# Optimization experiments

Hardware: AMD Instinct MI355X
Metric: run time of the kernel (lower is better)

Reference implementation:

```python
import jax, jax.numpy as jnp
import numpy as np

N = 32          # objects in the (single) image
P = N * (N - 1) # relation pairs
D = 256         # self.dim
M = 14          # mask_size / pooler resolution
OC = 151        # obj classes
RC = 51         # rel classes
RED = D // 4    # attention gate reduction


def setup_inputs() -> dict:
    key = jax.random.key(0)
    ks = jax.random.split(key, 32)
    # all ordered pairs i != j
    ii, jj = np.meshgrid(np.arange(N), np.arange(N), indexing='ij')
    keep = ii != jj
    rel_pair_idxs = jnp.asarray(np.stack([ii[keep], jj[keep]], 1), jnp.int32)  # [P,2]
    # valid xyxy boxes in an 800x600 image
    x1 = jax.random.uniform(ks[0], (N,)) * 600.0
    y1 = jax.random.uniform(ks[1], (N,)) * 400.0
    w = jax.random.uniform(ks[2], (N,)) * 180.0 + 20.0
    h = jax.random.uniform(ks[3], (N,)) * 180.0 + 20.0
    bboxes = jnp.stack([x1, y1, x1 + w, y1 + h], 1).astype(jnp.float32)
    roi_features = jax.random.normal(ks[4], (N, 4096), jnp.float32)
    predict_logits = jax.random.normal(ks[5], (N, OC), jnp.float32)
    union_features = jax.random.normal(ks[6], (P, D, M, M), jnp.float32)
    s = 0.02
    p = dict(
        roi_features=roi_features, bboxes=bboxes, predict_logits=predict_logits,
        union_features=union_features, rel_pair_idxs=rel_pair_idxs,
        W_emb1=jax.random.normal(ks[7], (4096 + OC + 4, D)) * s, b_emb1=jnp.zeros((D,)),
        W_emb2=jax.random.normal(ks[8], (D, D)) * s, b_emb2=jnp.zeros((D,)),
        # stacked SE-attention gates: 0=sbj, 1=obj, 2=bg
        att_fc1_w=jax.random.normal(ks[9], (3, D, RED)) * s, att_fc1_b=jnp.zeros((3, RED)),
        att_fc2_w=jax.random.normal(ks[10], (3, RED, D)) * s, att_fc2_b=jnp.zeros((3, D)),
        W_c1=jax.random.normal(ks[11], (3 * D, D)) * s, b_c1=jnp.zeros((D,)),
        W_c2=jax.random.normal(ks[12], (D, D)) * s, b_c2=jnp.zeros((D,)),
        W_gcn=jax.random.normal(ks[13], (D, D)) * s, b_gcn=jnp.zeros((D,)),
        W_objp=jax.random.normal(ks[14], (D, OC)) * s, b_objp=jnp.zeros((OC,)),
        W_relp=jax.random.normal(ks[15], (D, RC)) * s, b_relp=jnp.zeros((RC,)),
    )
    return p


def _rect_masks(x0, y0, x1, y1):
    # mask[p, r, c] = 1 iff x0<=r<x1 and y0<=c<y1  (matches torch slice write)
    r = jnp.arange(M, dtype=jnp.float32)
    rm = (r[None, :] >= x0[:, None]) & (r[None, :] < x1[:, None])  # [P,M]
    cm = (r[None, :] >= y0[:, None]) & (r[None, :] < y1[:, None])  # [P,M]
    return (rm[:, :, None] & cm[:, None, :]).astype(jnp.float32)   # [P,M,M]


def _masking(union_features, bboxes, pairs):
    sb = bboxes[pairs[:, 0]]  # [P,4]
    ob = bboxes[pairs[:, 1]]
    ux1 = jnp.minimum(sb[:, 0], ob[:, 0])
    uy1 = jnp.minimum(sb[:, 1], ob[:, 1])
    x = jnp.stack([sb[:, 0], sb[:, 2], ob[:, 0], ob[:, 2]], 1) - ux1[:, None]
    y = jnp.stack([sb[:, 1], sb[:, 3], ob[:, 1], ob[:, 3]], 1) - uy1[:, None]
    xr = M / jnp.maximum(x[:, 1], x[:, 3])
    yr = M / jnp.maximum(y[:, 1], y[:, 3])
    xp = jnp.round(x * xr[:, None])
    yp = jnp.round(y * yr[:, None])
    sm = _rect_masks(xp[:, 0], yp[:, 0], xp[:, 1], yp[:, 1])[:, None]  # [P,1,M,M]
    om = _rect_masks(xp[:, 2], yp[:, 2], xp[:, 3], yp[:, 3])[:, None]
    bm = jnp.clip(1.0 - sm - om, 0.0, 1.0)
    return union_features * sm, union_features * om, union_features * bm


def _att_gate(x, w1, b1, w2, b2):
    # SE-style channel attention gate
    s = x.mean((2, 3))                                        # [P,D]
    g = jax.nn.sigmoid(jax.nn.relu(s @ w1 + b1) @ w2 + b2)    # [P,D]
    return x * g[:, :, None, None]


def _adjacency(pairs):
    o2o = jnp.zeros((N, N)).at[pairs[:, 0], pairs[:, 1]].set(1.0)
    ar = jnp.arange(P)
    o2r = jnp.zeros((N, P)).at[pairs[:, 0], ar].set(1.0).at[pairs[:, 1], ar].set(1.0)
    top = jnp.concatenate([o2o, o2r], 1)                     # [N, N+P]
    bot = jnp.concatenate([o2r.T, jnp.zeros((P, P))], 1)     # [P, N+P]
    adj = jnp.concatenate([top, bot], 0)
    return adj + jnp.eye(N + P)


def reference(roi_features, bboxes, predict_logits, union_features, rel_pair_idxs,
              W_emb1, b_emb1, W_emb2, b_emb2,
              att_fc1_w, att_fc1_b, att_fc2_w, att_fc2_b,
              W_c1, b_c1, W_c2, b_c2, W_gcn, b_gcn,
              W_objp, b_objp, W_relp, b_relp):
    pairs = rel_pair_idxs
    # object embedding
    obj_in = jnp.concatenate([roi_features, predict_logits, bboxes], 1)  # [N,4251]
    obj_feats = jax.nn.relu(obj_in @ W_emb1 + b_emb1) @ W_emb2 + b_emb2  # [N,D]
    # masking + attention gates + global avg pool
    sbj, obj, bg = _masking(union_features, bboxes, pairs)
    sbj = _att_gate(sbj, att_fc1_w[0], att_fc1_b[0], att_fc2_w[0], att_fc2_b[0]).mean((2, 3))
    obj = _att_gate(obj, att_fc1_w[1], att_fc1_b[1], att_fc2_w[1], att_fc2_b[1]).mean((2, 3))
    bg = _att_gate(bg, att_fc1_w[2], att_fc1_b[2], att_fc2_w[2], att_fc2_b[2]).mean((2, 3))
    # relational embedding (compose)
    rel = jnp.concatenate([sbj, obj, bg], 1)                 # [P,3D]
    rel_feats = jax.nn.relu(rel @ W_c1 + b_c1) @ W_c2 + b_c2  # [P,D]
    # GCN over object+relation graph (row-normalized adjacency, residual)
    adj = _adjacency(pairs)
    feats = jnp.concatenate([obj_feats, rel_feats], 0)        # [N+P,D]
    norm_adj = adj / adj.sum(1, keepdims=True)
    gcn_out = jax.nn.relu(norm_adj @ (feats @ W_gcn) + b_gcn) + feats
    obj_dists = gcn_out[:N] @ W_objp + b_objp                 # [N,OC]
    rel_dists = gcn_out[N:] @ W_relp + b_relp                 # [P,RC]
    return obj_dists, rel_dists
```

## Files before the change

### kernel.cpp

```cpp
#include <hip/hip_runtime.h>
#include <cstdint>
#include <cstddef>

#define NOBJ 32
#define NP   992
#define DD   256
#define SP   196
#define OC   151
#define RC   51
#define RED  64
#define KIN  4251
#define CH   128
#define KPC  34

#define OFF_PART   0u
#define OFF_OBJF   1048576u
#define OFF_SALL   1056768u
#define OFF_RELF   1818624u
#define OFF_H      2072576u
#define OFF_W2T    2334720u
#define OFF_WC1T   2400256u
#define OFF_WC2T   2596864u
#define OFF_WGT    2662400u
#define OFF_FC1WT  2727936u
#define OFF_FC2WT  2777088u
#define OFF_WOPT   2826240u
#define OFF_WRPT   2864896u

#define TR_TOT 543232

#define TCH  32
#define NTIL 8
#define TF4  1568

__global__ void __launch_bounds__(256, 5)
k_pre(const float* __restrict__ uf,
      const float* __restrict__ bbox,
      const int* __restrict__ pairs,
      const float* __restrict__ roi,
      const float* __restrict__ logits,
      const float* __restrict__ W1,
      const float* __restrict__ W2,  const float* __restrict__ Wc1,
      const float* __restrict__ Wc2, const float* __restrict__ Wg,
      const float* __restrict__ f1w, const float* __restrict__ f2w,
      const float* __restrict__ Wop, const float* __restrict__ Wrp,
      float* __restrict__ sAll, float* __restrict__ part,
      float* __restrict__ W2T,  float* __restrict__ Wc1T,
      float* __restrict__ Wc2T, float* __restrict__ WgT,
      float* __restrict__ f1wT, float* __restrict__ f2wT,
      float* __restrict__ WopT, float* __restrict__ WrpT) {
  const int b = blockIdx.x, t = threadIdx.x;
  if (b < NP) {
    const int p = b;
    __shared__ __align__(16) float buf[TCH * SP + 28];
    __shared__ __align__(16) float mS[224];
    __shared__ __align__(16) float mO[224];
    __shared__ __align__(16) float mB[224];
    if (t < 224) {
      float sm = 0.f, om = 0.f, bm = 0.f;
      if (t < SP) {
        int si = pairs[2 * p], oi = pairs[2 * p + 1];
        float sx1 = bbox[si * 4 + 0], sy1 = bbox[si * 4 + 1];
        float sx2 = bbox[si * 4 + 2], sy2 = bbox[si * 4 + 3];
        float ox1 = bbox[oi * 4 + 0], oy1 = bbox[oi * 4 + 1];
        float ox2 = bbox[oi * 4 + 2], oy2 = bbox[oi * 4 + 3];
        float ux = fminf(sx1, ox1), uy = fminf(sy1, oy1);
        float xr = 14.f / fmaxf(sx2 - ux, ox2 - ux);
        float yr = 14.f / fmaxf(sy2 - uy, oy2 - uy);
        float xs0 = rintf((sx1 - ux) * xr), xs1 = rintf((sx2 - ux) * xr);
        float xo0 = rintf((ox1 - ux) * xr), xo1 = rintf((ox2 - ux) * xr);
        float ys0 = rintf((sy1 - uy) * yr), ys1 = rintf((sy2 - uy) * yr);
        float yo0 = rintf((oy1 - uy) * yr), yo1 = rintf((oy2 - uy) * yr);
        int a = t / 14, bb = t - a * 14;
        float fa = (float)a, fb = (float)bb;
        sm = (fa >= xs0 && fa < xs1 && fb >= ys0 && fb < ys1) ? 1.f : 0.f;
        om = (fa >= xo0 && fa < xo1 && fb >= yo0 && fb < yo1) ? 1.f : 0.f;
        bm = fminf(fmaxf(1.f - sm - om, 0.f), 1.f);
      }
      mS[t] = sm; mO[t] = om; mB[t] = bm;
    }
    if (t < 28) buf[TCH * SP + t] = 0.f;
    const float4* base4 = (const float4*)(uf + (size_t)p * (DD * SP));
    {
      const float4* src = base4 + t;
      float4* dst = (float4*)buf + t;
      dst[0] = src[0];     dst[256] = src[256];   dst[512] = src[512];
      dst[768] = src[768]; dst[1024] = src[1024]; dst[1280] = src[1280];
      if (t < 32) dst[1536] = src[1536];
    }
    __syncthreads();
    const int cl = t >> 3, o = t & 7;
    const float* row = buf + cl * SP + o * 28;
    const float* msp = mS + o * 28;
    const float* mop = mO + o * 28;
    const float* mbp = mB + o * 28;
    const float inv = 1.f / 196.f;
    float4 s0, s1, s2, s3, s4, s5, s6 = {0.f, 0.f, 0.f, 0.f};
#pragma unroll 1
    for (int ti = 0; ti < NTIL; ++ti) {
      if (ti < NTIL - 1) {
        const float4* src = base4 + (ti + 1) * TF4 + t;
        s0 = src[0];     s1 = src[256];   s2 = src[512];
        s3 = src[768];   s4 = src[1024];  s5 = src[1280];
        if (t < 32) s6 = src[1536];
      }
      float aS = 0.f, aO = 0.f, aB = 0.f;
#pragma unroll
      for (int j = 0; j < 7; ++j) {
        float4 v = *(const float4*)&row[4 * j];
        float4 x = *(const float4*)&msp[4 * j];
        float4 y = *(const float4*)&mop[4 * j];
        float4 z = *(const float4*)&mbp[4 * j];
        aS += v.x * x.x + v.y * x.y + v.z * x.z + v.w * x.w;
        aO += v.x * y.x + v.y * y.y + v.z * y.z + v.w * y.w;
        aB += v.x * z.x + v.y * z.y + v.z * z.z + v.w * z.w;
      }
      aS += __shfl_xor(aS, 1); aS += __shfl_xor(aS, 2); aS += __shfl_xor(aS, 4);
      aO += __shfl_xor(aO, 1); aO += __shfl_xor(aO, 2); aO += __shfl_xor(aO, 4);
      aB += __shfl_xor(aB, 1); aB += __shfl_xor(aB, 2); aB += __shfl_xor(aB, 4);
      const int ch = ti * TCH + cl;
      if (o == 0)      sAll[(size_t)p * 768 + ch]       = aS * inv;
      else if (o == 1) sAll[(size_t)p * 768 + 256 + ch] = aO * inv;
      else if (o == 2) sAll[(size_t)p * 768 + 512 + ch] = aB * inv;
      if (ti < NTIL - 1) {
        __syncthreads();
        float4* dst = (float4*)buf + t;
        dst[0] = s0;     dst[256] = s1;   dst[512] = s2;
        dst[768] = s3;   dst[1024] = s4;  dst[1280] = s5;
        if (t < 32) dst[1536] = s6;
        __syncthreads();
      }
    }
  } else if (b < NP + CH) {
    const int chunk = b - NP;
    int k0 = chunk * KPC;
    int k1 = k0 + KPC; if (k1 > KIN) k1 = KIN;
    float acc[NOBJ];
#pragma unroll
    for (int i = 0; i < NOBJ; ++i) acc[i] = 0.f;
#pragma unroll 2
    for (int k = k0; k < k1; ++k) {
      float w = W1[(size_t)k * DD + t];
      const float* xp; int stride;
      if (k < 4096)            { xp = roi    + k;               stride = 4096; }
      else if (k < 4096 + OC)  { xp = logits + (k - 4096);      stride = OC;   }
      else                     { xp = bbox   + (k - 4096 - OC); stride = 4;    }
#pragma unroll
      for (int i = 0; i < NOBJ; ++i) { acc[i] += xp[0] * w; xp += stride; }
    }
    float* pout = part + (size_t)chunk * (NOBJ * DD) + t;
#pragma unroll
    for (int i = 0; i < NOBJ; ++i) pout[i * DD] = acc[i];
  } else {
    for (int o = (b - NP - CH) * 256 + t; o < TR_TOT; o += 256 * 256) {
      float v; float* dst;
      if (o < 65536)       { int q = o;          v = W2 [(q & 255) * 256 + (q >> 8)]; dst = W2T  + q; }
      else if (o < 262144) { int q = o - 65536;  int c = q / 768, k = q - c * 768;
                             v = Wc1[k * 256 + c];                                    dst = Wc1T + q; }
      else if (o < 327680) { int q = o - 262144; v = Wc2[(q & 255) * 256 + (q >> 8)]; dst = Wc2T + q; }
      else if (o < 393216) { int q = o - 327680; v = Wg [(q & 255) * 256 + (q >> 8)]; dst = WgT  + q; }
      else if (o < 442368) { int q = o - 393216;
                             v = f1w[(q >> 14) * 16384 + (q & 255) * 64 + ((q >> 8) & 63)];
                             dst = f1wT + q; }
      else if (o < 491520) { int q = o - 442368;
                             v = f2w[(q >> 14) * 16384 + (q & 63) * 256 + ((q >> 6) & 255)];
                             dst = f2wT + q; }
      else if (o < 530176) { int q = o - 491520; v = Wop[(q & 255) * OC + (q >> 8)];  dst = WopT + q; }
      else                 { int q = o - 530176; v = Wrp[(q & 255) * RC + (q >> 8)];  dst = WrpT + q; }
      *dst = v;
    }
  }
}

__global__ void __launch_bounds__(512, 1)
k_mid2(const float* __restrict__ sAll,
       const float* __restrict__ f1wT, const float* __restrict__ f1b,
       const float* __restrict__ f2wT, const float* __restrict__ f2b,
       const float* __restrict__ Wc1T, const float* __restrict__ bc1,
       const float* __restrict__ Wc2T, const float* __restrict__ bc2,
       const float* __restrict__ WgT,
       const float* __restrict__ part, const float* __restrict__ b1,
       const float* __restrict__ W2T,  const float* __restrict__ b2,
       float* __restrict__ relf, float* __restrict__ objf,
       float* __restrict__ H) {
  const int b = blockIdx.x, t = threadIdx.x;
  const int h = t >> 8, tt = t & 255;
  __shared__ __align__(16) float sg[4][768];
  __shared__ __align__(16) float ha[4][192];
  __shared__ __align__(16) float h2[4][256];
  __shared__ __align__(16) float red[2][4][256];
  if (b < NP / 4) {
    const int p0 = b * 4;
    {
      const float4* src = (const float4*)(sAll + (size_t)p0 * 768);
      float4* dst = (float4*)&sg[0][0];
      for (int j = t; j < 768; j += 512) dst[j] = src[j];
    }
    __syncthreads();
    if (tt < 192) {
      const float4* w4 = (const float4*)(f1wT + tt * 256 + h * 128);
      const int sb = (tt >> 6) * 256 + h * 128;
      float a0 = 0, a1 = 0, a2 = 0, a3 = 0;
#pragma unroll 8
      for (int j = 0; j < 32; ++j) {
        float4 wv = w4[j];
        float4 s0 = *(const float4*)&sg[0][sb + 4 * j];
        float4 s1 = *(const float4*)&sg[1][sb + 4 * j];
        float4 s2 = *(const float4*)&sg[2][sb + 4 * j];
        float4 s3 = *(const float4*)&sg[3][sb + 4 * j];
        a0 += s0.x * wv.x + s0.y * wv.y + s0.z * wv.z + s0.w * wv.w;
        a1 += s1.x * wv.x + s1.y * wv.y + s1.z * wv.z + s1.w * wv.w;
        a2 += s2.x * wv.x + s2.y * wv.y + s2.z * wv.z + s2.w * wv.w;
        a3 += s3.x * wv.x + s3.y * wv.y + s3.z * wv.z + s3.w * wv.w;
      }
      red[h][0][tt] = a0; red[h][1][tt] = a1; red[h][2][tt] = a2; red[h][3][tt] = a3;
    }
    __syncthreads();
    if (h == 0 && tt < 192) {
      float bb = f1b[tt];
#pragma unroll
      for (int p = 0; p < 4; ++p)
        ha[p][tt] = fmaxf(red[0][p][tt] + red[1][p][tt] + bb, 0.f);
    }
    __syncthreads();
    for (int br = 0; br < 3; ++br) {
      const float4* w4 = (const float4*)(f2wT + br * 16384 + tt * 64 + h * 32);
      const int hb = br * 64 + h * 32;
      float a0 = 0, a1 = 0, a2 = 0, a3 = 0;
#pragma unroll
      for (int j = 0; j < 8; ++j) {
        float4 wv = w4[j];
        float4 v0 = *(const float4*)&ha[0][hb + 4 * j];
        float4 v1 = *(const float4*)&ha[1][hb + 4 * j];
        float4 v2 = *(const float4*)&ha[2][hb + 4 * j];
        float4 v3 = *(const float4*)&ha[3][hb + 4 * j];
        a0 += v0.x * wv.x + v0.y * wv.y + v0.z * wv.z + v0.w * wv.w;
        a1 += v1.x * wv.x + v1.y * wv.y + v1.z * wv.z + v1.w * wv.w;
        a2 += v2.x * wv.x + v2.y * wv.y + v2.z * wv.z + v2.w * wv.w;
        a3 += v3.x * wv.x + v3.y * wv.y + v3.z * wv.z + v3.w * wv.w;
      }
      red[h][0][tt] = a0; red[h][1][tt] = a1; red[h][2][tt] = a2; red[h][3][tt] = a3;
      __syncthreads();
      if (h == 0) {
        float bb = f2b[br * 256 + tt];
#pragma unroll
        for (int p = 0; p < 4; ++p) {
          float g = 1.f / (1.f + expf(-(red[0][p][tt] + red[1][p][tt] + bb)));
          sg[p][br * 256 + tt] *= g;
        }
      }
      __syncthreads();
    }
    {
      const float4* w4 = (const float4*)(Wc1T + (size_t)tt * 768 + h * 384);
      const int gb = h * 384;
      float a0 = 0, a1 = 0, a2 = 0, a3 = 0;
#pragma unroll 8
      for (int j = 0; j < 96; ++j) {
        float4 wv = w4[j];
        float4 g0 = *(const float4*)&sg[0][gb + 4 * j];
        float4 g1 = *(const float4*)&sg[1][gb + 4 * j];
        float4 g2 = *(const float4*)&sg[2][gb + 4 * j];
        float4 g3 = *(const float4*)&sg[3][gb + 4 * j];
        a0 += g0.x * wv.x + g0.y * wv.y + g0.z * wv.z + g0.w * wv.w;
        a1 += g1.x * wv.x + g1.y * wv.y + g1.z * wv.z + g1.w * wv.w;
        a2 += g2.x * wv.x + g2.y * wv.y + g2.z * wv.z + g2.w * wv.w;
        a3 += g3.x * wv.x + g3.y * wv.y + g3.z * wv.z + g3.w * wv.w;
      }
      red[h][0][tt] = a0; red[h][1][tt] = a1; red[h][2][tt] = a2; red[h][3][tt] = a3;
    }
    __syncthreads();
    if (h == 0) {
      float bb = bc1[tt];
#pragma unroll
      for (int p = 0; p < 4; ++p)
        h2[p][tt] = fmaxf(red[0][p][tt] + red[1][p][tt] + bb, 0.f);
    }
    __syncthreads();
    {
      const float4* w4 = (const float4*)(Wc2T + (size_t)tt * 256 + h * 128);
      const int hb = h * 128;
      float a0 = 0, a1 = 0, a2 = 0, a3 = 0;
#pragma unroll 8
      for (int j = 0; j < 32; ++j) {
        float4 wv = w4[j];
        float4 v0 = *(const float4*)&h2[0][hb + 4 * j];
        float4 v1 = *(const float4*)&h2[1][hb + 4 * j];
        float4 v2 = *(const float4*)&h2[2][hb + 4 * j];
        float4 v3 = *(const float4*)&h2[3][hb + 4 * j];
        a0 += v0.x * wv.x + v0.y * wv.y + v0.z * wv.z + v0.w * wv.w;
        a1 += v1.x * wv.x + v1.y * wv.y + v1.z * wv.z + v1.w * wv.w;
        a2 += v2.x * wv.x + v2.y * wv.y + v2.z * wv.z + v2.w * wv.w;
        a3 += v3.x * wv.x + v3.y * wv.y + v3.z * wv.z + v3.w * wv.w;
      }
      red[h][0][tt] = a0; red[h][1][tt] = a1; red[h][2][tt] = a2; red[h][3][tt] = a3;
    }
    __syncthreads();
    if (h == 0) {
      float bb = bc2[tt];
#pragma unroll
      for (int p = 0; p < 4; ++p) {
        float v = red[0][p][tt] + red[1][p][tt] + bb;
        relf[(size_t)(p0 + p) * DD + tt] = v;
        sg[p][tt] = v;
      }
    }
    __syncthreads();
    {
      const float4* w4 = (const float4*)(WgT + (size_t)tt * 256 + h * 128);
      const int hb = h * 128;
      float a0 = 0, a1 = 0, a2 = 0, a3 = 0;
#pragma unroll 8
      for (int j = 0; j < 32; ++j) {
        float4 wv = w4[j];
        float4 v0 = *(const float4*)&sg[0][hb + 4 * j];
        float4 v1 = *(const float4*)&sg[1][hb + 4 * j];
        float4 v2 = *(const float4*)&sg[2][hb + 4 * j];
        float4 v3 = *(const float4*)&sg[3][hb + 4 * j];
        a0 += v0.x * wv.x + v0.y * wv.y + v0.z * wv.z + v0.w * wv.w;
        a1 += v1.x * wv.x + v1.y * wv.y + v1.z * wv.z + v1.w * wv.w;
        a2 += v2.x * wv.x + v2.y * wv.y + v2.z * wv.z + v2.w * wv.w;
        a3 += v3.x * wv.x + v3.y * wv.y + v3.z * wv.z + v3.w * wv.w;
      }
      red[h][0][tt] = a0; red[h][1][tt] = a1; red[h][2][tt] = a2; red[h][3][tt] = a3;
    }
    __syncthreads();
    if (h == 0) {
#pragma unroll
      for (int p = 0; p < 4; ++p)
        H[(size_t)(NOBJ + p0 + p) * DD + tt] = red[0][p][tt] + red[1][p][tt];
    }
  } else {
    const int r = (b - NP / 4) * 2 + h;
    float s[8];
#pragma unroll
    for (int u = 0; u < 8; ++u) s[u] = 0.f;
#pragma unroll
    for (int c0 = 0; c0 < CH; c0 += 8) {
#pragma unroll
      for (int u = 0; u < 8; ++u)
        s[u] += part[(size_t)(c0 + u) * (NOBJ * DD) + r * DD + tt];
    }
    float tot = ((s[0] + s[1]) + (s[2] + s[3])) + ((s[4] + s[5]) + (s[6] + s[7]));
    h2[h][tt] = fmaxf(tot + b1[tt], 0.f);
    __syncthreads();
    {
      const float4* w4 = (const float4*)(W2T + (size_t)tt * DD);
      const float* hp = &h2[h][0];
      float a0 = 0, a1 = 0, a2 = 0, a3 = 0;
#pragma unroll 8
      for (int j = 0; j < 64; ++j) {
        float4 wv = w4[j];
        float4 hv = *(const float4*)&hp[4 * j];
        a0 += hv.x * wv.x; a1 += hv.y * wv.y; a2 += hv.z * wv.z; a3 += hv.w * wv.w;
      }
      float v = (a0 + a1) + (a2 + a3) + b2[tt];
      objf[r * DD + tt] = v;
      sg[h][tt] = v;
    }
    __syncthreads();
    {
      const float4* w4 = (const float4*)(WgT + (size_t)tt * DD);
      const float* hp = &sg[h][0];
      float a0 = 0, a1 = 0, a2 = 0, a3 = 0;
#pragma unroll 8
      for (int j = 0; j < 64; ++j) {
        float4 wv = w4[j];
        float4 hv = *(const float4*)&hp[4 * j];
        a0 += hv.x * wv.x; a1 += hv.y * wv.y; a2 += hv.z * wv.z; a3 += hv.w * wv.w;
      }
      H[(size_t)r * DD + tt] = (a0 + a1) + (a2 + a3);
    }
  }
}

__global__ void __launch_bounds__(1024, 1)
k_heads(const float* __restrict__ H, const float* __restrict__ objf,
        const float* __restrict__ relf, const int* __restrict__ pairs,
        const float* __restrict__ bg,
        const float* __restrict__ WopT, const float* __restrict__ bop,
        const float* __restrict__ WrpT, const float* __restrict__ brp,
        float* __restrict__ out) {
  const int b = blockIdx.x, t = threadIdx.x;
  const int p = t >> 8, tt = t & 255;
  if (b < NP / 4) {
    __shared__ __align__(16) float gr[4][DD];
    __shared__ float red[4][4][64];
    const int r = b * 4 + p;
    int si = pairs[2 * r], oi = pairs[2 * r + 1];
    float hsum = H[si * DD + tt] + H[oi * DD + tt] + H[(size_t)(NOBJ + r) * DD + tt];
    gr[p][tt] = fmaxf(hsum * (1.f / 3.f) + bg[tt], 0.f) + relf[(size_t)r * DD + tt];
    __syncthreads();
    const int q = tt >> 6, c = tt & 63;
    float a = 0.f;
    if (c < RC) {
      const float4* w4 = (const float4*)(WrpT + c * 256 + q * 64);
#pragma unroll
      for (int j = 0; j < 16; ++j) {
        float4 wv = w4[j];
        float4 gv = *(const float4*)&gr[p][q * 64 + 4 * j];
        a += gv.x * wv.x + gv.y * wv.y + gv.z * wv.z + gv.w * wv.w;
      }
    }
    red[p][q][c] = a;
    __syncthreads();
    if (tt < RC)
      out[NOBJ * OC + (size_t)r * RC + tt] =
          red[p][0][tt] + red[p][1][tt] + red[p][2][tt] + red[p][3][tt] + brp[tt];
  } else {
    const int i = b - NP / 4;
    const int slice = p;
    __shared__ int2 pr[NP];
    __shared__ float red2[4][DD];
    __shared__ __align__(16) float gro[DD];
    const int2* p2 = (const int2*)pairs;
    for (int r = t; r < NP; r += 1024) pr[r] = p2[r];
    __syncthreads();
    float acc = 0.f;
    if (slice == 0) {
#pragma unroll 8
      for (int j = 0; j < NOBJ; ++j) acc += H[j * DD + tt];
    }
    const int rbeg = slice * 248;
#pragma unroll 8
    for (int r = rbeg; r < rbeg + 248; ++r) {
      int2 q = pr[r];
      float v = H[(size_t)(NOBJ + r) * DD + tt];
      if (q.x == i || q.y == i) acc += v;
    }
    red2[slice][tt] = acc;
    __syncthreads();
    if (t < DD) {
      float pre = (red2[0][t] + red2[1][t] + red2[2][t] + red2[3][t]) * (1.f / 94.f);
      gro[t] = fmaxf(pre + bg[t], 0.f) + objf[i * DD + t];
    }
    __syncthreads();
    float hsum = 0.f;
    if (tt < OC) {
      const float4* w4 = (const float4*)(WopT + tt * 256 + slice * 64);
#pragma unroll
      for (int j = 0; j < 16; ++j) {
        float4 wv = w4[j];
        float4 gv = *(const float4*)&gro[slice * 64 + 4 * j];
        hsum += gv.x * wv.x + gv.y * wv.y + gv.z * wv.z + gv.w * wv.w;
      }
    }
    red2[slice][tt] = hsum;
    __syncthreads();
    if (t < OC)
      out[i * OC + t] = red2[0][t] + red2[1][t] + red2[2][t] + red2[3][t] + bop[t];
  }
}

extern "C" void kernel_launch(void* const* d_in, const int* in_sizes, int n_in,
                              void* d_out, int out_size, void* d_ws, size_t ws_size,
                              hipStream_t stream) {
  const float* roi   = (const float*)d_in[0];
  const float* bbox  = (const float*)d_in[1];
  const float* logit = (const float*)d_in[2];
  const float* uf    = (const float*)d_in[3];
  const int*   pairs = (const int*)d_in[4];
  const float* W1    = (const float*)d_in[5];
  const float* b1    = (const float*)d_in[6];
  const float* W2    = (const float*)d_in[7];
  const float* b2    = (const float*)d_in[8];
  const float* fc1w  = (const float*)d_in[9];
  const float* fc1b  = (const float*)d_in[10];
  const float* fc2w  = (const float*)d_in[11];
  const float* fc2b  = (const float*)d_in[12];
  const float* Wc1   = (const float*)d_in[13];
  const float* bc1   = (const float*)d_in[14];
  const float* Wc2   = (const float*)d_in[15];
  const float* bc2   = (const float*)d_in[16];
  const float* Wg    = (const float*)d_in[17];
  const float* bg    = (const float*)d_in[18];
  const float* Wop   = (const float*)d_in[19];
  const float* bop   = (const float*)d_in[20];
  const float* Wrp   = (const float*)d_in[21];
  const float* brp   = (const float*)d_in[22];

  float* ws    = (float*)d_ws;
  float* part  = ws + OFF_PART;
  float* objf  = ws + OFF_OBJF;
  float* sAll  = ws + OFF_SALL;
  float* relf  = ws + OFF_RELF;
  float* Hbuf  = ws + OFF_H;
  float* W2T   = ws + OFF_W2T;
  float* Wc1T  = ws + OFF_WC1T;
  float* Wc2T  = ws + OFF_WC2T;
  float* WgT   = ws + OFF_WGT;
  float* f1wT  = ws + OFF_FC1WT;
  float* f2wT  = ws + OFF_FC2WT;
  float* WopT  = ws + OFF_WOPT;
  float* WrpT  = ws + OFF_WRPT;
  float* out   = (float*)d_out;

  k_pre<<<NP + CH + 256, 256, 0, stream>>>(uf, bbox, pairs, roi, logit, W1,
                                           W2, Wc1, Wc2, Wg, fc1w, fc2w, Wop, Wrp,
                                           sAll, part, W2T, Wc1T, Wc2T, WgT,
                                           f1wT, f2wT, WopT, WrpT);
  k_mid2<<<NP / 4 + 16, 512, 0, stream>>>(sAll, f1wT, fc1b, f2wT, fc2b,
                                          Wc1T, bc1, Wc2T, bc2, WgT,
                                          part, b1, W2T, b2, relf, objf, Hbuf);
  k_heads<<<NP / 4 + NOBJ, 1024, 0, stream>>>(Hbuf, objf, relf, pairs, bg,
                                              WopT, bop, WrpT, brp, out);
}
```

Measured before the change: 498.6 us.

## Read union features directly from global memory instead of LDS staging

The masked-pooling phase stops staging each pair's union-feature tile into shared memory with a register-prefetch double buffer. Each group of four threads now reduces one channel row straight from global memory with float4 loads, and the reduction shuffle shrinks from three levels to two. This removes about 25 KB of LDS per block and the barriers between tiles, which should allow higher occupancy and remove the sync overhead. In exchange, the global loads are strided per channel and less coalesced, and there is no explicit prefetch. The launch-bounds occupancy hint drops from 5 to 4.

```diff
diff --git a/kernel.cpp b/kernel.cpp
--- a/kernel.cpp
+++ b/kernel.cpp
@@ -29,11 +29,7 @@
 
 #define TR_TOT 543232
 
-#define TCH  32
-#define NTIL 8
-#define TF4  1568
-
-__global__ void __launch_bounds__(256, 5)
+__global__ void __launch_bounds__(256, 4)
 k_pre(const float* __restrict__ uf,
       const float* __restrict__ bbox,
       const int* __restrict__ pairs,
@@ -52,7 +48,6 @@
   const int b = blockIdx.x, t = threadIdx.x;
   if (b < NP) {
     const int p = b;
-    __shared__ __align__(16) float buf[TCH * SP + 28];
     __shared__ __align__(16) float mS[224];
     __shared__ __align__(16) float mO[224];
     __shared__ __align__(16) float mB[224];
@@ -79,57 +74,42 @@
       }
       mS[t] = sm; mO[t] = om; mB[t] = bm;
     }
-    if (t < 28) buf[TCH * SP + t] = 0.f;
-    const float4* base4 = (const float4*)(uf + (size_t)p * (DD * SP));
-    {
-      const float4* src = base4 + t;
-      float4* dst = (float4*)buf + t;
-      dst[0] = src[0];     dst[256] = src[256];   dst[512] = src[512];
-      dst[768] = src[768]; dst[1024] = src[1024]; dst[1280] = src[1280];
-      if (t < 32) dst[1536] = src[1536];
-    }
-    __syncthreads();
-    const int cl = t >> 3, o = t & 7;
-    const float* row = buf + cl * SP + o * 28;
-    const float* msp = mS + o * 28;
-    const float* mop = mO + o * 28;
-    const float* mbp = mB + o * 28;
+    __syncthreads();
+    const int g = t >> 2, i = t & 3;
     const float inv = 1.f / 196.f;
-    float4 s0, s1, s2, s3, s4, s5, s6 = {0.f, 0.f, 0.f, 0.f};
+    const float* base = uf + (size_t)p * (DD * SP);
+    const size_t pout = (size_t)p * 768;
 #pragma unroll 1
-    for (int ti = 0; ti < NTIL; ++ti) {
-      if (ti < NTIL - 1) {
-        const float4* src = base4 + (ti + 1) * TF4 + t;
-        s0 = src[0];     s1 = src[256];   s2 = src[512];
-        s3 = src[768];   s4 = src[1024];  s5 = src[1280];
-        if (t < 32) s6 = src[1536];
-      }
+    for (int c0 = 0; c0 < DD; c0 += 64) {
+      const int c = c0 + g;
+      const float* row = base + c * SP;
       float aS = 0.f, aO = 0.f, aB = 0.f;
 #pragma unroll
-      for (int j = 0; j < 7; ++j) {
-        float4 v = *(const float4*)&row[4 * j];
-        float4 x = *(const float4*)&msp[4 * j];
-        float4 y = *(const float4*)&mop[4 * j];
-        float4 z = *(const float4*)&mbp[4 * j];
+      for (int j = 0; j < 12; ++j) {
+        const int q = 4 * j + i;
+        float4 v = *(const float4*)(row + 4 * q);
+        float4 x = *(const float4*)&mS[4 * q];
+        float4 y = *(const float4*)&mO[4 * q];
+        float4 z = *(const float4*)&mB[4 * q];
         aS += v.x * x.x + v.y * x.y + v.z * x.z + v.w * x.w;
         aO += v.x * y.x + v.y * y.y + v.z * y.z + v.w * y.w;
         aB += v.x * z.x + v.y * z.y + v.z * z.z + v.w * z.w;
       }
-      aS += __shfl_xor(aS, 1); aS += __shfl_xor(aS, 2); aS += __shfl_xor(aS, 4);
-      aO += __shfl_xor(aO, 1); aO += __shfl_xor(aO, 2); aO += __shfl_xor(aO, 4);
-      aB += __shfl_xor(aB, 1); aB += __shfl_xor(aB, 2); aB += __shfl_xor(aB, 4);
-      const int ch = ti * TCH + cl;
-      if (o == 0)      sAll[(size_t)p * 768 + ch]       = aS * inv;
-      else if (o == 1) sAll[(size_t)p * 768 + 256 + ch] = aO * inv;
-      else if (o == 2) sAll[(size_t)p * 768 + 512 + ch] = aB * inv;
-      if (ti < NTIL - 1) {
-        __syncthreads();
-        float4* dst = (float4*)buf + t;
-        dst[0] = s0;     dst[256] = s1;   dst[512] = s2;
-        dst[768] = s3;   dst[1024] = s4;  dst[1280] = s5;
-        if (t < 32) dst[1536] = s6;
-        __syncthreads();
-      }
+      if (i == 0) {
+        float4 v = *(const float4*)(row + 192);
+        float4 x = *(const float4*)&mS[192];
+        float4 y = *(const float4*)&mO[192];
+        float4 z = *(const float4*)&mB[192];
+        aS += v.x * x.x + v.y * x.y + v.z * x.z + v.w * x.w;
+        aO += v.x * y.x + v.y * y.y + v.z * y.z + v.w * y.w;
+        aB += v.x * z.x + v.y * z.y + v.z * z.z + v.w * z.w;
+      }
+      aS += __shfl_xor(aS, 1); aS += __shfl_xor(aS, 2);
+      aO += __shfl_xor(aO, 1); aO += __shfl_xor(aO, 2);
+      aB += __shfl_xor(aB, 1); aB += __shfl_xor(aB, 2);
+      if (i == 0)      sAll[pout + c]       = aS * inv;
+      else if (i == 1) sAll[pout + 256 + c] = aO * inv;
+      else if (i == 2) sAll[pout + 512 + c] = aB * inv;
     }
   } else if (b < NP + CH) {
     const int chunk = b - NP;
```

Measured after the change: 539.8 us. 1.08x slower.

## Read weights in native layout in k_mid2, drop transpose pre-pass

Applied to the files above, without the earlier changes.

Removes the transpose of most dense weights (W2, Wc1, Wc2, Wg, gate fc1/fc2) from k_pre. k_mid2 now reads those weights in their original row-major layout, with coalesced float4 column reads per lane. Work is remapped so each 64-lane wavefront owns one relation pair, with 256-thread blocks instead of 512 and no cross-half reduction buffer. This cuts transpose traffic and the extra workspace writes and reads, but each wavefront now re-reads every weight matrix for a single pair, so weight reuse per block drops.

```diff
diff --git a/kernel.cpp b/kernel.cpp
--- a/kernel.cpp
+++ b/kernel.cpp
@@ -27,7 +27,7 @@
 #define OFF_WOPT   2826240u
 #define OFF_WRPT   2864896u
 
-#define TR_TOT 543232
+#define TR_TOT 51712
 
 #define TCH  32
 #define NTIL 8
@@ -40,14 +40,8 @@
       const float* __restrict__ roi,
       const float* __restrict__ logits,
       const float* __restrict__ W1,
-      const float* __restrict__ W2,  const float* __restrict__ Wc1,
-      const float* __restrict__ Wc2, const float* __restrict__ Wg,
-      const float* __restrict__ f1w, const float* __restrict__ f2w,
       const float* __restrict__ Wop, const float* __restrict__ Wrp,
       float* __restrict__ sAll, float* __restrict__ part,
-      float* __restrict__ W2T,  float* __restrict__ Wc1T,
-      float* __restrict__ Wc2T, float* __restrict__ WgT,
-      float* __restrict__ f1wT, float* __restrict__ f2wT,
       float* __restrict__ WopT, float* __restrict__ WrpT) {
   const int b = blockIdx.x, t = threadIdx.x;
   if (b < NP) {
@@ -152,186 +146,143 @@
 #pragma unroll
     for (int i = 0; i < NOBJ; ++i) pout[i * DD] = acc[i];
   } else {
-    for (int o = (b - NP - CH) * 256 + t; o < TR_TOT; o += 256 * 256) {
+    for (int o = (b - NP - CH) * 256 + t; o < TR_TOT; o += 64 * 256) {
       float v; float* dst;
-      if (o < 65536)       { int q = o;          v = W2 [(q & 255) * 256 + (q >> 8)]; dst = W2T  + q; }
-      else if (o < 262144) { int q = o - 65536;  int c = q / 768, k = q - c * 768;
-                             v = Wc1[k * 256 + c];                                    dst = Wc1T + q; }
-      else if (o < 327680) { int q = o - 262144; v = Wc2[(q & 255) * 256 + (q >> 8)]; dst = Wc2T + q; }
-      else if (o < 393216) { int q = o - 327680; v = Wg [(q & 255) * 256 + (q >> 8)]; dst = WgT  + q; }
-      else if (o < 442368) { int q = o - 393216;
-                             v = f1w[(q >> 14) * 16384 + (q & 255) * 64 + ((q >> 8) & 63)];
-                             dst = f1wT + q; }
-      else if (o < 491520) { int q = o - 442368;
-                             v = f2w[(q >> 14) * 16384 + (q & 63) * 256 + ((q >> 6) & 255)];
-                             dst = f2wT + q; }
-      else if (o < 530176) { int q = o - 491520; v = Wop[(q & 255) * OC + (q >> 8)];  dst = WopT + q; }
-      else                 { int q = o - 530176; v = Wrp[(q & 255) * RC + (q >> 8)];  dst = WrpT + q; }
+      if (o < 38656) { int q = o;         v = Wop[(q & 255) * OC + (q >> 8)]; dst = WopT + q; }
+      else           { int q = o - 38656; v = Wrp[(q & 255) * RC + (q >> 8)]; dst = WrpT + q; }
       *dst = v;
     }
   }
 }
 
-__global__ void __launch_bounds__(512, 1)
+__global__ void __launch_bounds__(256, 4)
 k_mid2(const float* __restrict__ sAll,
-       const float* __restrict__ f1wT, const float* __restrict__ f1b,
-       const float* __restrict__ f2wT, const float* __restrict__ f2b,
-       const float* __restrict__ Wc1T, const float* __restrict__ bc1,
-       const float* __restrict__ Wc2T, const float* __restrict__ bc2,
-       const float* __restrict__ WgT,
+       const float* __restrict__ f1w, const float* __restrict__ f1b,
+       const float* __restrict__ f2w, const float* __restrict__ f2b,
+       const float* __restrict__ Wc1, const float* __restrict__ bc1,
+       const float* __restrict__ Wc2, const float* __restrict__ bc2,
+       const float* __restrict__ Wg,
        const float* __restrict__ part, const float* __restrict__ b1,
-       const float* __restrict__ W2T,  const float* __restrict__ b2,
+       const float* __restrict__ W2,  const float* __restrict__ b2,
        float* __restrict__ relf, float* __restrict__ objf,
        float* __restrict__ H) {
   const int b = blockIdx.x, t = threadIdx.x;
-  const int h = t >> 8, tt = t & 255;
   __shared__ __align__(16) float sg[4][768];
   __shared__ __align__(16) float ha[4][192];
   __shared__ __align__(16) float h2[4][256];
-  __shared__ __align__(16) float red[2][4][256];
+  __shared__ __align__(16) float hob[256];
+  __shared__ __align__(16) float eob[256];
   if (b < NP / 4) {
-    const int p0 = b * 4;
-    {
-      const float4* src = (const float4*)(sAll + (size_t)p0 * 768);
-      float4* dst = (float4*)&sg[0][0];
-      for (int j = t; j < 768; j += 512) dst[j] = src[j];
-    }
-    __syncthreads();
-    if (tt < 192) {
-      const float4* w4 = (const float4*)(f1wT + tt * 256 + h * 128);
-      const int sb = (tt >> 6) * 256 + h * 128;
-      float a0 = 0, a1 = 0, a2 = 0, a3 = 0;
+    const int w = t >> 6, l = t & 63;
+    const int r = b * 4 + w;
+    {
+      const float4* src = (const float4*)(sAll + (size_t)r * 768);
+      float4* dst = (float4*)&sg[w][0];
+      dst[l] = src[l]; dst[64 + l] = src[64 + l]; dst[128 + l] = src[128 + l];
+    }
+    __syncthreads();
+    {
+      float a0 = 0.f, a1 = 0.f, a2 = 0.f;
+      const float* w0 = f1w + l;
+      const float* w1 = f1w + 16384 + l;
+      const float* w2 = f1w + 32768 + l;
+#pragma unroll 4
+      for (int d4 = 0; d4 < 64; ++d4) {
+        float4 x0 = *((const float4*)&sg[w][0]   + d4);
+        float4 x1 = *((const float4*)&sg[w][256] + d4);
+        float4 x2 = *((const float4*)&sg[w][512] + d4);
+        int d = 4 * d4;
+        a0 += x0.x * w0[d * 64] + x0.y * w0[(d + 1) * 64] +
+              x0.z * w0[(d + 2) * 64] + x0.w * w0[(d + 3) * 64];
+        a1 += x1.x * w1[d * 64] + x1.y * w1[(d + 1) * 64] +
+              x1.z * w1[(d + 2) * 64] + x1.w * w1[(d + 3) * 64];
+        a2 += x2.x * w2[d * 64] + x2.y * w2[(d + 1) * 64] +
+              x2.z * w2[(d + 2) * 64] + x2.w * w2[(d + 3) * 64];
+      }
+      ha[w][l]       = fmaxf(a0 + f1b[l], 0.f);
+      ha[w][64 + l]  = fmaxf(a1 + f1b[64 + l], 0.f);
+      ha[w][128 + l] = fmaxf(a2 + f1b[128 + l], 0.f);
+    }
+    __syncthreads();
+#pragma unroll
+    for (int br = 0; br < 3; ++br) {
+      float ax = 0.f, ay = 0.f, az = 0.f, aw = 0.f;
+      const float4* wp = (const float4*)(f2w + br * 16384) + l;
 #pragma unroll 8
-      for (int j = 0; j < 32; ++j) {
-        float4 wv = w4[j];
-        float4 s0 = *(const float4*)&sg[0][sb + 4 * j];
-        float4 s1 = *(const float4*)&sg[1][sb + 4 * j];
-        float4 s2 = *(const float4*)&sg[2][sb + 4 * j];
-        float4 s3 = *(const float4*)&sg[3][sb + 4 * j];
-        a0 += s0.x * wv.x + s0.y * wv.y + s0.z * wv.z + s0.w * wv.w;
-        a1 += s1.x * wv.x + s1.y * wv.y + s1.z * wv.z + s1.w * wv.w;
-        a2 += s2.x * wv.x + s2.y * wv.y + s2.z * wv.z + s2.w * wv.w;
-        a3 += s3.x * wv.x + s3.y * wv.y + s3.z * wv.z + s3.w * wv.w;
-      }
-      red[h][0][tt] = a0; red[h][1][tt] = a1; red[h][2][tt] = a2; red[h][3][tt] = a3;
-    }
-    __syncthreads();
-    if (h == 0 && tt < 192) {
-      float bb = f1b[tt];
-#pragma unroll
-      for (int p = 0; p < 4; ++p)
-        ha[p][tt] = fmaxf(red[0][p][tt] + red[1][p][tt] + bb, 0.f);
-    }
-    __syncthreads();
-    for (int br = 0; br < 3; ++br) {
-      const float4* w4 = (const float4*)(f2wT + br * 16384 + tt * 64 + h * 32);
-      const int hb = br * 64 + h * 32;
-      float a0 = 0, a1 = 0, a2 = 0, a3 = 0;
-#pragma unroll
-      for (int j = 0; j < 8; ++j) {
-        float4 wv = w4[j];
-        float4 v0 = *(const float4*)&ha[0][hb + 4 * j];
-        float4 v1 = *(const float4*)&ha[1][hb + 4 * j];
-        float4 v2 = *(const float4*)&ha[2][hb + 4 * j];
-        float4 v3 = *(const float4*)&ha[3][hb + 4 * j];
-        a0 += v0.x * wv.x + v0.y * wv.y + v0.z * wv.z + v0.w * wv.w;
-        a1 += v1.x * wv.x + v1.y * wv.y + v1.z * wv.z + v1.w * wv.w;
-        a2 += v2.x * wv.x + v2.y * wv.y + v2.z * wv.z + v2.w * wv.w;
-        a3 += v3.x * wv.x + v3.y * wv.y + v3.z * wv.z + v3.w * wv.w;
-      }
-      red[h][0][tt] = a0; red[h][1][tt] = a1; red[h][2][tt] = a2; red[h][3][tt] = a3;
-      __syncthreads();
-      if (h == 0) {
-        float bb = f2b[br * 256 + tt];
-#pragma unroll
-        for (int p = 0; p < 4; ++p) {
-          float g = 1.f / (1.f + expf(-(red[0][p][tt] + red[1][p][tt] + bb)));
-          sg[p][br * 256 + tt] *= g;
-        }
-      }
-      __syncthreads();
-    }
-    {
-      const float4* w4 = (const float4*)(Wc1T + (size_t)tt * 768 + h * 384);
-      const int gb = h * 384;
-      float a0 = 0, a1 = 0, a2 = 0, a3 = 0;
-#pragma unroll 8
-      for (int j = 0; j < 96; ++j) {
-        float4 wv = w4[j];
-        float4 g0 = *(const float4*)&sg[0][gb + 4 * j];
-        float4 g1 = *(const float4*)&sg[1][gb + 4 * j];
-        float4 g2 = *(const float4*)&sg[2][gb + 4 * j];
-        float4 g3 = *(const float4*)&sg[3][gb + 4 * j];
-        a0 += g0.x * wv.x + g0.y * wv.y + g0.z * wv.z + g0.w * wv.w;
-        a1 += g1.x * wv.x + g1.y * wv.y + g1.z * wv.z + g1.w * wv.w;
-        a2 += g2.x * wv.x + g2.y * wv.y + g2.z * wv.z + g2.w * wv.w;
-        a3 += g3.x * wv.x + g3.y * wv.y + g3.z * wv.z + g3.w * wv.w;
-      }
-      red[h][0][tt] = a0; red[h][1][tt] = a1; red[h][2][tt] = a2; red[h][3][tt] = a3;
-    }
-    __syncthreads();
-    if (h == 0) {
-      float bb = bc1[tt];
-#pragma unroll
-      for (int p = 0; p < 4; ++p)
-        h2[p][tt] = fmaxf(red[0][p][tt] + red[1][p][tt] + bb, 0.f);
-    }
-    __syncthreads();
-    {
-      const float4* w4 = (const float4*)(Wc2T + (size_t)tt * 256 + h * 128);
-      const int hb = h * 128;
-      float a0 = 0, a1 = 0, a2 = 0, a3 = 0;
-#pragma unroll 8
-      for (int j = 0; j < 32; ++j) {
-        float4 wv = w4[j];
-        float4 v0 = *(const float4*)&h2[0][hb + 4 * j];
-        float4 v1 = *(const float4*)&h2[1][hb + 4 * j];
-        float4 v2 = *(const float4*)&h2[2][hb + 4 * j];
-        float4 v3 = *(const float4*)&h2[3][hb + 4 * j];
-        a0 += v0.x * wv.x + v0.y * wv.y + v0.z * wv.z + v0.w * wv.w;
-        a1 += v1.x * wv.x + v1.y * wv.y + v1.z * wv.z + v1.w * wv.w;
-        a2 += v2.x * wv.x + v2.y * wv.y + v2.z * wv.z + v2.w * wv.w;
-        a3 += v3.x * wv.x + v3.y * wv.y + v3.z * wv.z + v3.w * wv.w;
-      }
-      red[h][0][tt] = a0; red[h][1][tt] = a1; red[h][2][tt] = a2; red[h][3][tt] = a3;
-    }
-    __syncthreads();
-    if (h == 0) {
-      float bb = bc2[tt];
-#pragma unroll
-      for (int p = 0; p < 4; ++p) {
-        float v = red[0][p][tt] + red[1][p][tt] + bb;
-        relf[(size_t)(p0 + p) * DD + tt] = v;
-        sg[p][tt] = v;
-      }
-    }
-    __syncthreads();
-    {
-      const float4* w4 = (const float4*)(WgT + (size_t)tt * 256 + h * 128);
-      const int hb = h * 128;
-      float a0 = 0, a1 = 0, a2 = 0, a3 = 0;
-#pragma unroll 8
-      for (int j = 0; j < 32; ++j) {
-        float4 wv = w4[j];
-        float4 v0 = *(const float4*)&sg[0][hb + 4 * j];
-        float4 v1 = *(const float4*)&sg[1][hb + 4 * j];
-        float4 v2 = *(const float4*)&sg[2][hb + 4 * j];
-        float4 v3 = *(const float4*)&sg[3][hb + 4 * j];
-        a0 += v0.x * wv.x + v0.y * wv.y + v0.z * wv.z + v0.w * wv.w;
-        a1 += v1.x * wv.x + v1.y * wv.y + v1.z * wv.z + v1.w * wv.w;
-        a2 += v2.x * wv.x + v2.y * wv.y + v2.z * wv.z + v2.w * wv.w;
-        a3 += v3.x * wv.x + v3.y * wv.y + v3.z * wv.z + v3.w * wv.w;
-      }
-      red[h][0][tt] = a0; red[h][1][tt] = a1; red[h][2][tt] = a2; red[h][3][tt] = a3;
-    }
-    __syncthreads();
-    if (h == 0) {
-#pragma unroll
-      for (int p = 0; p < 4; ++p)
-        H[(size_t)(NOBJ + p0 + p) * DD + tt] = red[0][p][tt] + red[1][p][tt];
+      for (int red = 0; red < 64; ++red) {
+        float x = ha[w][br * 64 + red];
+        float4 wv = wp[red * 64];
+        ax += x * wv.x; ay += x * wv.y; az += x * wv.z; aw += x * wv.w;
+      }
+      float4 bb = *((const float4*)(f2b + br * 256) + l);
+      float4 sv = *((float4*)&sg[w][br * 256] + l);
+      sv.x *= 1.f / (1.f + expf(-(ax + bb.x)));
+      sv.y *= 1.f / (1.f + expf(-(ay + bb.y)));
+      sv.z *= 1.f / (1.f + expf(-(az + bb.z)));
+      sv.w *= 1.f / (1.f + expf(-(aw + bb.w)));
+      *((float4*)&sg[w][br * 256] + l) = sv;
+    }
+    __syncthreads();
+    {
+      float ax = 0.f, ay = 0.f, az = 0.f, aw = 0.f;
+      const float4* wp = (const float4*)Wc1 + l;
+#pragma unroll 4
+      for (int k4 = 0; k4 < 192; ++k4) {
+        float4 x = *((const float4*)&sg[w][0] + k4);
+        int k = 4 * k4;
+        float4 v0 = wp[(size_t)k * 64], v1 = wp[(size_t)(k + 1) * 64];
+        float4 v2 = wp[(size_t)(k + 2) * 64], v3 = wp[(size_t)(k + 3) * 64];
+        ax += x.x * v0.x + x.y * v1.x + x.z * v2.x + x.w * v3.x;
+        ay += x.x * v0.y + x.y * v1.y + x.z * v2.y + x.w * v3.y;
+        az += x.x * v0.z + x.y * v1.z + x.z * v2.z + x.w * v3.z;
+        aw += x.x * v0.w + x.y * v1.w + x.z * v2.w + x.w * v3.w;
+      }
+      float4 bb = *((const float4*)bc1 + l);
+      float4 hv;
+      hv.x = fmaxf(ax + bb.x, 0.f); hv.y = fmaxf(ay + bb.y, 0.f);
+      hv.z = fmaxf(az + bb.z, 0.f); hv.w = fmaxf(aw + bb.w, 0.f);
+      *((float4*)&h2[w][0] + l) = hv;
+    }
+    __syncthreads();
+    {
+      float ax = 0.f, ay = 0.f, az = 0.f, aw = 0.f;
+      const float4* wp = (const float4*)Wc2 + l;
+#pragma unroll 4
+      for (int k4 = 0; k4 < 64; ++k4) {
+        float4 x = *((const float4*)&h2[w][0] + k4);
+        int k = 4 * k4;
+        float4 v0 = wp[k * 64], v1 = wp[(k + 1) * 64];
+        float4 v2 = wp[(k + 2) * 64], v3 = wp[(k + 3) * 64];
+        ax += x.x * v0.x + x.y * v1.x + x.z * v2.x + x.w * v3.x;
+        ay += x.x * v0.y + x.y * v1.y + x.z * v2.y + x.w * v3.y;
+        az += x.x * v0.z + x.y * v1.z + x.z * v2.z + x.w * v3.z;
+        aw += x.x * v0.w + x.y * v1.w + x.z * v2.w + x.w * v3.w;
+      }
+      float4 bb = *((const float4*)bc2 + l);
+      float4 v; v.x = ax + bb.x; v.y = ay + bb.y; v.z = az + bb.z; v.w = aw + bb.w;
+      *(float4*)(relf + (size_t)r * DD + 4 * l) = v;
+      *((float4*)&sg[w][0] + l) = v;
+    }
+    __syncthreads();
+    {
+      float ax = 0.f, ay = 0.f, az = 0.f, aw = 0.f;
+      const float4* wp = (const float4*)Wg + l;
+#pragma unroll 4
+      for (int k4 = 0; k4 < 64; ++k4) {
+        float4 x = *((const float4*)&sg[w][0] + k4);
+        int k = 4 * k4;
+        float4 v0 = wp[k * 64], v1 = wp[(k + 1) * 64];
+        float4 v2 = wp[(k + 2) * 64], v3 = wp[(k + 3) * 64];
+        ax += x.x * v0.x + x.y * v1.x + x.z * v2.x + x.w * v3.x;
+        ay += x.x * v0.y + x.y * v1.y + x.z * v2.y + x.w * v3.y;
+        az += x.x * v0.z + x.y * v1.z + x.z * v2.z + x.w * v3.z;
+        aw += x.x * v0.w + x.y * v1.w + x.z * v2.w + x.w * v3.w;
+      }
+      float4 v; v.x = ax; v.y = ay; v.z = az; v.w = aw;
+      *(float4*)(H + (size_t)(NOBJ + r) * DD + 4 * l) = v;
     }
   } else {
-    const int r = (b - NP / 4) * 2 + h;
+    const int i = b - NP / 4;
     float s[8];
 #pragma unroll
     for (int u = 0; u < 8; ++u) s[u] = 0.f;
@@ -339,37 +290,35 @@
     for (int c0 = 0; c0 < CH; c0 += 8) {
 #pragma unroll
       for (int u = 0; u < 8; ++u)
-        s[u] += part[(size_t)(c0 + u) * (NOBJ * DD) + r * DD + tt];
+        s[u] += part[(size_t)(c0 + u) * (NOBJ * DD) + i * DD + t];
     }
     float tot = ((s[0] + s[1]) + (s[2] + s[3])) + ((s[4] + s[5]) + (s[6] + s[7]));
-    h2[h][tt] = fmaxf(tot + b1[tt], 0.f);
-    __syncthreads();
-    {
-      const float4* w4 = (const float4*)(W2T + (size_t)tt * DD);
-      const float* hp = &h2[h][0];
-      float a0 = 0, a1 = 0, a2 = 0, a3 = 0;
-#pragma unroll 8
-      for (int j = 0; j < 64; ++j) {
-        float4 wv = w4[j];
-        float4 hv = *(const float4*)&hp[4 * j];
-        a0 += hv.x * wv.x; a1 += hv.y * wv.y; a2 += hv.z * wv.z; a3 += hv.w * wv.w;
-      }
-      float v = (a0 + a1) + (a2 + a3) + b2[tt];
-      objf[r * DD + tt] = v;
-      sg[h][tt] = v;
-    }
-    __syncthreads();
-    {
-      const float4* w4 = (const float4*)(WgT + (size_t)tt * DD);
-      const float* hp = &sg[h][0];
-      float a0 = 0, a1 = 0, a2 = 0, a3 = 0;
-#pragma unroll 8
-      for (int j = 0; j < 64; ++j) {
-        float4 wv = w4[j];
-        float4 hv = *(const float4*)&hp[4 * j];
-        a0 += hv.x * wv.x; a1 += hv.y * wv.y; a2 += hv.z * wv.z; a3 += hv.w * wv.w;
-      }
-      H[(size_t)r * DD + tt] = (a0 + a1) + (a2 + a3);
+    hob[t] = fmaxf(tot + b1[t], 0.f);
+    __syncthreads();
+    {
+      float a = 0.f;
+#pragma unroll 4
+      for (int k4 = 0; k4 < 64; ++k4) {
+        float4 hv = *((const float4*)hob + k4);
+        int k = 4 * k4;
+        a += hv.x * W2[k * 256 + t]       + hv.y * W2[(k + 1) * 256 + t]
+           + hv.z * W2[(k + 2) * 256 + t] + hv.w * W2[(k + 3) * 256 + t];
+      }
+      float v = a + b2[t];
+      objf[i * DD + t] = v;
+      eob[t] = v;
+    }
+    __syncthreads();
+    {
+      float a = 0.f;
+#pragma unroll 4
+      for (int k4 = 0; k4 < 64; ++k4) {
+        float4 ev = *((const float4*)eob + k4);
+        int k = 4 * k4;
+        a += ev.x * Wg[k * 256 + t]       + ev.y * Wg[(k + 1) * 256 + t]
+           + ev.z * Wg[(k + 2) * 256 + t] + ev.w * Wg[(k + 3) * 256 + t];
+      }
+      H[(size_t)i * DD + t] = a;
     }
   }
 }
@@ -485,23 +434,15 @@
   float* sAll  = ws + OFF_SALL;
   float* relf  = ws + OFF_RELF;
   float* Hbuf  = ws + OFF_H;
-  float* W2T   = ws + OFF_W2T;
-  float* Wc1T  = ws + OFF_WC1T;
-  float* Wc2T  = ws + OFF_WC2T;
-  float* WgT   = ws + OFF_WGT;
-  float* f1wT  = ws + OFF_FC1WT;
-  float* f2wT  = ws + OFF_FC2WT;
   float* WopT  = ws + OFF_WOPT;
   float* WrpT  = ws + OFF_WRPT;
   float* out   = (float*)d_out;
 
-  k_pre<<<NP + CH + 256, 256, 0, stream>>>(uf, bbox, pairs, roi, logit, W1,
-                                           W2, Wc1, Wc2, Wg, fc1w, fc2w, Wop, Wrp,
-                                           sAll, part, W2T, Wc1T, Wc2T, WgT,
-                                           f1wT, f2wT, WopT, WrpT);
-  k_mid2<<<NP / 4 + 16, 512, 0, stream>>>(sAll, f1wT, fc1b, f2wT, fc2b,
-                                          Wc1T, bc1, Wc2T, bc2, WgT,
-                                          part, b1, W2T, b2, relf, objf, Hbuf);
+  k_pre<<<NP + CH + 64, 256, 0, stream>>>(uf, bbox, pairs, roi, logit, W1,
+                                          Wop, Wrp, sAll, part, WopT, WrpT);
+  k_mid2<<<NP / 4 + NOBJ, 256, 0, stream>>>(sAll, fc1w, fc1b, fc2w, fc2b,
+                                            Wc1, bc1, Wc2, bc2, Wg,
+                                            part, b1, W2, b2, relf, objf, Hbuf);
   k_heads<<<NP / 4 + NOBJ, 1024, 0, stream>>>(Hbuf, objf, relf, pairs, bg,
                                               WopT, bop, WrpT, brp, out);
 }
```

Result: slower. 514.3 us (+3.1%).
